# Kernel tuning notes

Measured on AMD Instinct MI355X. Metric: run time of the kernel, lower is better.

The kernel has to match this reference:

```python
import jax, jax.numpy as jnp
import numpy as np
from jax import lax

BN_EPS = 1e-5

def _conv(x, w, b, stride=2, pad=1):
    y = lax.conv_general_dilated(x, w, (stride, stride), [(pad, pad), (pad, pad)],
                                 dimension_numbers=('NCHW', 'OIHW', 'NCHW'))
    return y + b[None, :, None, None]

def _leaky(x):
    return jnp.where(x >= 0, x, 0.2 * x)

def setup_inputs() -> dict:
    key = jax.random.key(0)
    ks = jax.random.split(key, 10)
    B, C, S = 64, 3, 128
    flat = 128 * (S // 4) * (S // 4)  # 131072
    out_f, kdims = 100, 5
    def kaiming(k, shape, fan_in):
        bound = 1.0 / np.sqrt(fan_in)
        return jax.random.uniform(k, shape, jnp.float32, -bound, bound)
    x = jax.random.normal(ks[0], (B, C, S, S), jnp.float32)
    conv1_w = kaiming(ks[1], (64, C, 4, 4), C * 16)
    conv1_b = kaiming(ks[2], (64,), C * 16)
    conv2_w = kaiming(ks[3], (128, 64, 4, 4), 64 * 16)
    conv2_b = kaiming(ks[4], (128,), 64 * 16)
    bn_gamma = jnp.ones((128,), jnp.float32)
    bn_beta = jnp.zeros((128,), jnp.float32)
    T = jax.random.normal(ks[5], (flat, out_f, kdims), jnp.float32)  # N(0,1) init
    lin_w = kaiming(ks[6], (1, flat + out_f), flat + out_f)
    lin_b = kaiming(ks[7], (1,), flat + out_f)
    return {"x": x, "conv1_w": conv1_w, "conv1_b": conv1_b,
            "conv2_w": conv2_w, "conv2_b": conv2_b,
            "bn_gamma": bn_gamma, "bn_beta": bn_beta,
            "T": T, "lin_w": lin_w, "lin_b": lin_b}

def reference(x, conv1_w, conv1_b, conv2_w, conv2_b, bn_gamma, bn_beta, T, lin_w, lin_b):
    B = x.shape[0]
    h = _leaky(_conv(x, conv1_w, conv1_b))          # [B,64,S/2,S/2]
    h = _conv(h, conv2_w, conv2_b)                  # [B,128,S/4,S/4]
    mu = jnp.mean(h, axis=(0, 2, 3), keepdims=True)  # batchnorm (train mode, batch stats)
    var = jnp.mean((h - mu) ** 2, axis=(0, 2, 3), keepdims=True)
    h = (h - mu) * lax.rsqrt(var + BN_EPS)
    h = h * bn_gamma[None, :, None, None] + bn_beta[None, :, None, None]
    h = _leaky(h)
    feat = h.reshape(B, -1)                          # [B, flat]
    # minibatch discrimination
    M = (feat @ T.reshape(T.shape[0], -1)).reshape(B, T.shape[1], T.shape[2])  # [B,out,k]
    norm = jnp.abs(M[None, :, :, :] - M[:, None, :, :]).sum(3)  # [B,B,out] pairwise L1
    o_b = jnp.exp(-norm).sum(0)                      # [B,out]
    feat = jnp.concatenate([feat, o_b], axis=1)      # [B, flat+out]
    logits = feat @ lin_w.T + lin_b
    return jax.nn.sigmoid(logits)                    # [B,1]
```

## Files before the change

kernel.cpp:

```cpp
#include <hip/hip_runtime.h>
#include <hip/hip_bf16.h>
#include <math.h>

#define BB 64
#define SS 128
#define C1 64
#define H1D 64
#define C2 128
#define H2D 32
#define FLAT 131072
#define NCOL 500
#define KCH 256
#define KCSZ 512

typedef __attribute__((ext_vector_type(4))) float f32x4;
typedef __attribute__((ext_vector_type(8))) short bf16x8;

__device__ inline float bf2f(short s) {
    union { unsigned int u; float f; } z;
    z.u = ((unsigned int)(unsigned short)s) << 16;
    return z.f;
}

__global__ __launch_bounds__(256) void k_conv1p(const float* __restrict__ x,
    const float* __restrict__ w, const float* __restrict__ bias,
    const float* __restrict__ w2,
    __hip_bfloat16* __restrict__ h1, __hip_bfloat16* __restrict__ Bw)
{
    int bid = blockIdx.x;
    if (bid < 512) {
      int i = bid*256 + threadIdx.x;
      int jj = i & 7, oc = (i>>3)&127, kl8 = (i>>10)&31, stage = i>>15;
      int kl = kl8*8 + jj;
      int tap = kl >> 4, icl = kl & 15;
      int ic = stage*16 + icl;
      Bw[i] = __float2bfloat16(w2[(size_t)oc*1024 + ic*16 + tap]);
      return;
    }
    int tid = (bid - 512)*256 + threadIdx.x;
    int ow = tid & 63, oh = (tid>>6)&63, bi = tid>>12;
    int ih0 = oh*2-1, iw0 = ow*2-1;
    float in[48];
    #pragma unroll
    for (int ic=0; ic<3; ic++)
      #pragma unroll
      for (int kh=0; kh<4; kh++)
        #pragma unroll
        for (int kw=0; kw<4; kw++) {
          int ih = ih0+kh, iw = iw0+kw;
          float v = 0.f;
          if ((unsigned)ih < 128u && (unsigned)iw < 128u)
            v = x[((size_t)(bi*3+ic)*SS + ih)*SS + iw];
          in[ic*16+kh*4+kw] = v;
        }
    #pragma unroll
    for (int g=0; g<4; g++) {
      __hip_bfloat16 outv[16];
      #pragma unroll
      for (int ocl=0; ocl<16; ocl++) {
        int oc = g*16 + ocl;
        float a = bias[oc];
        const float* wp = w + oc*48;
        #pragma unroll
        for (int t=0; t<48; t++) a = fmaf(in[t], wp[t], a);
        a = a >= 0.f ? a : 0.2f*a;
        outv[ocl] = __float2bfloat16(a);
      }
      __hip_bfloat16* dst = h1 + (((size_t)g*BB + bi)*4096 + oh*64 + ow)*16;
      *(bf16x8*)(dst)     = *(bf16x8*)&outv[0];
      *(bf16x8*)(dst + 8) = *(bf16x8*)&outv[8];
    }
}

__global__ __launch_bounds__(256) void k_conv2(const __hip_bfloat16* __restrict__ h1,
    const __hip_bfloat16* __restrict__ Bw, const float* __restrict__ b2,
    __hip_bfloat16* __restrict__ h2b, double* __restrict__ bnp2)
{
    int bid = blockIdx.x;
    int nh = (bid >> 3) & 1;
    int pair = (bid >> 4)*8 + (bid & 7);
    int bi = pair >> 2, strip = pair & 3;
    int lane = threadIdx.x & 63, wv = threadIdx.x >> 6;
    int l15 = lane & 15, kg = lane >> 4;

    __shared__ __align__(16) short tile[36*33*24];
    __shared__ float2 bnl[4][16][16];

    f32x4 acc[4][4];
    #pragma unroll
    for (int m=0;m<4;m++)
      #pragma unroll
      for (int n=0;n<4;n++) acc[m][n] = (f32x4)(0.f);

    int ihb = strip*16 - 1;

    for (int stage=0; stage<4; ++stage) {
      const __hip_bfloat16* hsrc = h1 + ((size_t)stage*BB + bi)*4096*16;
      for (int idx = threadIdx.x; idx < 2376; idx += 256) {
        int half = idx & 1, p = idx >> 1;
        int ih_l = p / 66, iw_l = p - ih_l*66;
        int ih = ihb + ih_l, iw = iw_l - 1;
        int row48 = (ih_l*2 + (iw_l&1))*33 + (iw_l>>1);
        bf16x8 v = (bf16x8)(0);
        if ((unsigned)ih < 64u && (unsigned)iw < 64u)
          v = *(const bf16x8*)(hsrc + ((size_t)(ih*64+iw)*16 + half*8));
        *(bf16x8*)&tile[row48*24 + half*8] = v;
      }
      __syncthreads();
      const __hip_bfloat16* bwst = Bw + (size_t)stage*32*128*8;
      #pragma unroll
      for (int j=0; j<8; j++) {
        bf16x8 bf[4];
        #pragma unroll
        for (int nf=0; nf<4; nf++)
          bf[nf] = *(const bf16x8*)(bwst + ((size_t)((j*4+kg)*128) + nh*64 + nf*16 + l15)*8);
        int tap = 2*j + (kg>>1);
        int kh = tap>>2, kw = tap&3;
        int icl0 = (kg&1)*8;
        bf16x8 af[4];
        #pragma unroll
        for (int mf=0; mf<4; mf++) {
          int oh_l = 2*wv + (mf>>1);
          int ow   = (mf&1)*16 + l15;
          int ih_l = 2*oh_l + kh;
          int iw_l = 2*ow + kw;
          int row48 = (ih_l*2 + (iw_l&1))*33 + (iw_l>>1);
          af[mf] = *(const bf16x8*)&tile[row48*24 + icl0];
        }
        #pragma unroll
        for (int mf=0; mf<4; mf++)
          #pragma unroll
          for (int nf=0; nf<4; nf++)
            acc[mf][nf] = __builtin_amdgcn_mfma_f32_16x16x32_bf16(af[mf], bf[nf], acc[mf][nf], 0, 0, 0);
      }
      __syncthreads();
    }
    #pragma unroll
    for (int nf=0; nf<4; nf++) {
      int oc = nh*64 + nf*16 + l15;
      float bv = b2[oc];
      float s1 = 0.f, s2 = 0.f;
      #pragma unroll
      for (int mf=0; mf<4; mf++) {
        int p0 = wv*64 + mf*16 + kg*4;
        float v0 = acc[mf][nf][0] + bv;
        float v1 = acc[mf][nf][1] + bv;
        float v2 = acc[mf][nf][2] + bv;
        float v3 = acc[mf][nf][3] + bv;
        s1 += v0+v1+v2+v3;
        s2 = fmaf(v0,v0, fmaf(v1,v1, fmaf(v2,v2, fmaf(v3,v3, s2))));
        __hip_bfloat16 o4[4];
        o4[0] = __float2bfloat16(v0); o4[1] = __float2bfloat16(v1);
        o4[2] = __float2bfloat16(v2); o4[3] = __float2bfloat16(v3);
        *(double*)&h2b[((size_t)bi*C2 + oc)*1024 + strip*256 + p0] = *(double*)o4;
      }
      bnl[nf][wv*4+kg][l15] = make_float2(s1, s2);
    }
    __syncthreads();
    if (threadIdx.x < 64) {
      int nf = threadIdx.x >> 4, l = threadIdx.x & 15;
      double s1 = 0.0, s2 = 0.0;
      #pragma unroll
      for (int i=0;i<16;i++) {
        float2 v = bnl[nf][i][l];
        s1 += (double)v.x; s2 += (double)v.y;
      }
      int oc = nh*64 + nf*16 + l;
      bnp2[(size_t)oc*256 + pair]         = s1;
      bnp2[32768 + (size_t)oc*256 + pair] = s2;
    }
}

__global__ __launch_bounds__(256) void k_bnred(const double* __restrict__ bnp2,
    const float* __restrict__ gamma, const float* __restrict__ beta,
    float* __restrict__ stats)
{
    int c = blockIdx.x;
    int p = threadIdx.x;
    double s1 = bnp2[(size_t)c*256 + p];
    double s2 = bnp2[32768 + (size_t)c*256 + p];
    __shared__ double r1[256], r2[256];
    r1[p] = s1; r2[p] = s2;
    __syncthreads();
    for (int st = 128; st > 0; st >>= 1) {
      if (p < st) { r1[p] += r1[p+st]; r2[p] += r2[p+st]; }
      __syncthreads();
    }
    if (p == 0) {
      double mean = r1[0] * (1.0/65536.0);
      double var  = r2[0] * (1.0/65536.0) - mean*mean;
      double rstd = 1.0 / sqrt(var + 1e-5);
      double sc = rstd * (double)gamma[c];
      stats[c]       = (float)sc;
      stats[C2 + c]  = (float)((double)beta[c] - mean*sc);
    }
}

__global__ __launch_bounds__(256) void k_mgemm(const __hip_bfloat16* __restrict__ h2b,
    const float* __restrict__ stats, const float* __restrict__ T,
    __hip_bfloat16* __restrict__ Mpart)
{
    int t = threadIdx.x;
    int lane = t & 63, wv = t >> 6;
    int l15 = lane & 15, kg = lane >> 4;
    int bid = blockIdx.x;
    int xc = bid & 7, j = bid >> 3;
    int kc = xc*32 + (j >> 2);
    int ng = j & 3;
    int k0b = kc * KCSZ;

    int ch = kc >> 1;
    float sc = stats[ch], sh = stats[C2 + ch];

    __shared__ float Ts[2][32][134];

    int f4c = t & 31, rbase = t >> 5;
    int cols4 = ng*128 + f4c*4;
    bool cvalid = cols4 < 500;

    f32x4 acc[4][2];
    #pragma unroll
    for (int m=0;m<4;m++) { acc[m][0] = (f32x4)(0.f); acc[m][1] = (f32x4)(0.f); }

    float4 tv0, tv1, tv2, tv3;
    {
      int ks0 = k0b;
      tv0 = cvalid ? *(const float4*)&T[(size_t)(ks0+rbase   )*NCOL + cols4] : make_float4(0,0,0,0);
      tv1 = cvalid ? *(const float4*)&T[(size_t)(ks0+rbase+ 8)*NCOL + cols4] : make_float4(0,0,0,0);
      tv2 = cvalid ? *(const float4*)&T[(size_t)(ks0+rbase+16)*NCOL + cols4] : make_float4(0,0,0,0);
      tv3 = cvalid ? *(const float4*)&T[(size_t)(ks0+rbase+24)*NCOL + cols4] : make_float4(0,0,0,0);
      float* d0 = &Ts[0][rbase   ][f4c*4];
      float* d1 = &Ts[0][rbase+ 8][f4c*4];
      float* d2 = &Ts[0][rbase+16][f4c*4];
      float* d3 = &Ts[0][rbase+24][f4c*4];
      *(float2*)d0 = make_float2(tv0.x,tv0.y); *(float2*)(d0+2) = make_float2(tv0.z,tv0.w);
      *(float2*)d1 = make_float2(tv1.x,tv1.y); *(float2*)(d1+2) = make_float2(tv1.z,tv1.w);
      *(float2*)d2 = make_float2(tv2.x,tv2.y); *(float2*)(d2+2) = make_float2(tv2.z,tv2.w);
      *(float2*)d3 = make_float2(tv3.x,tv3.y); *(float2*)(d3+2) = make_float2(tv3.z,tv3.w);
    }
    __syncthreads();

    for (int s = 0; s < 16; s++) {
      int cur = s & 1;
      if (s < 15) {
        int ks0 = k0b + (s+1)*32;
        tv0 = cvalid ? *(const float4*)&T[(size_t)(ks0+rbase   )*NCOL + cols4] : make_float4(0,0,0,0);
        tv1 = cvalid ? *(const float4*)&T[(size_t)(ks0+rbase+ 8)*NCOL + cols4] : make_float4(0,0,0,0);
        tv2 = cvalid ? *(const float4*)&T[(size_t)(ks0+rbase+16)*NCOL + cols4] : make_float4(0,0,0,0);
        tv3 = cvalid ? *(const float4*)&T[(size_t)(ks0+rbase+24)*NCOL + cols4] : make_float4(0,0,0,0);
      }
      {
        int k0 = k0b + s*32;
        bf16x8 af[4];
        #pragma unroll
        for (int mf=0; mf<4; mf++) {
          bf16x8 raw = *(const bf16x8*)(h2b + (size_t)(mf*16 + l15)*FLAT + k0 + kg*8);
          __hip_bfloat16 ta[8];
          #pragma unroll
          for (int jj=0; jj<8; jj++) {
            float f = fmaf(bf2f(raw[jj]), sc, sh);
            f = f >= 0.f ? f : 0.2f*f;
            ta[jj] = __float2bfloat16(f);
          }
          af[mf] = *(bf16x8*)ta;
        }
        bf16x8 bfr[2];
        #pragma unroll
        for (int nf=0; nf<2; nf++) {
          int c = wv*32 + nf*16 + l15;
          __hip_bfloat16 tb[8];
          #pragma unroll
          for (int jj=0; jj<8; jj++)
            tb[jj] = __float2bfloat16(Ts[cur][kg*8+jj][c]);
          bfr[nf] = *(bf16x8*)tb;
        }
        #pragma unroll
        for (int mf=0;mf<4;mf++)
          #pragma unroll
          for (int nf=0;nf<2;nf++)
            acc[mf][nf] = __builtin_amdgcn_mfma_f32_16x16x32_bf16(af[mf], bfr[nf], acc[mf][nf], 0, 0, 0);
      }
      __syncthreads();
      if (s < 15) {
        int nb = cur ^ 1;
        float* d0 = &Ts[nb][rbase   ][f4c*4];
        float* d1 = &Ts[nb][rbase+ 8][f4c*4];
        float* d2 = &Ts[nb][rbase+16][f4c*4];
        float* d3 = &Ts[nb][rbase+24][f4c*4];
        *(float2*)d0 = make_float2(tv0.x,tv0.y); *(float2*)(d0+2) = make_float2(tv0.z,tv0.w);
        *(float2*)d1 = make_float2(tv1.x,tv1.y); *(float2*)(d1+2) = make_float2(tv1.z,tv1.w);
        *(float2*)d2 = make_float2(tv2.x,tv2.y); *(float2*)(d2+2) = make_float2(tv2.z,tv2.w);
        *(float2*)d3 = make_float2(tv3.x,tv3.y); *(float2*)(d3+2) = make_float2(tv3.z,tv3.w);
        __syncthreads();
      }
    }
    __hip_bfloat16* op = Mpart + (size_t)(kc*4 + ng)*8192;
    #pragma unroll
    for (int mf=0; mf<4; mf++) {
      __hip_bfloat16 buf[8];
      #pragma unroll
      for (int nf=0; nf<2; nf++)
        #pragma unroll
        for (int q=0; q<4; q++)
          buf[nf*4+q] = __float2bfloat16(acc[mf][nf][q]);
      *(bf16x8*)(op + ((size_t)mf*256 + t)*8) = *(bf16x8*)buf;
    }
}

__global__ __launch_bounds__(256) void k_mreduceA(const __hip_bfloat16* __restrict__ Mpart,
    float* __restrict__ Mpart2)
{
    int ng = blockIdx.x & 3, kg8 = blockIdx.x >> 2;
    int t = threadIdx.x;
    f32x4 a0[4], a1[4];
    #pragma unroll
    for (int mf=0; mf<4; mf++) { a0[mf] = (f32x4)(0.f); a1[mf] = (f32x4)(0.f); }
    #pragma unroll
    for (int kcl=0; kcl<8; kcl++) {
      int kc = kg8*8 + kcl;
      const __hip_bfloat16* ch = Mpart + (size_t)(kc*4 + ng)*8192;
      #pragma unroll
      for (int mf=0; mf<4; mf++) {
        bf16x8 v = *(const bf16x8*)(ch + ((size_t)mf*256 + t)*8);
        a0[mf][0] += bf2f(v[0]); a0[mf][1] += bf2f(v[1]);
        a0[mf][2] += bf2f(v[2]); a0[mf][3] += bf2f(v[3]);
        a1[mf][0] += bf2f(v[4]); a1[mf][1] += bf2f(v[5]);
        a1[mf][2] += bf2f(v[6]); a1[mf][3] += bf2f(v[7]);
      }
    }
    #pragma unroll
    for (int mf=0; mf<4; mf++) {
      float* dst = Mpart2 + ((size_t)(ng*32 + kg8)*4 + mf)*2048 + t*8;
      *(f32x4*)dst = a0[mf];
      *(f32x4*)(dst+4) = a1[mf];
    }
}

__global__ __launch_bounds__(256) void k_ob(const float* __restrict__ Mpart2,
    float* __restrict__ ob)
{
    int o = blockIdx.x;
    __shared__ float Ms[320];
    __shared__ float red[256];
    for (int idx = threadIdx.x; idx < 320; idx += 256) {
      int a = idx / 5, d = idx - a*5;
      int r = a, c = o*5 + d;
      int mf = r >> 4, kg = (r >> 2) & 3, q = r & 3;
      int ng = c >> 7, wv = (c >> 5) & 3, nf = (c >> 4) & 1, l15 = c & 15;
      int t = wv*64 + kg*16 + l15, j8 = nf*4 + q;
      const float* p = Mpart2 + ((size_t)(ng*32)*4 + mf)*2048 + t*8 + j8;
      float s = 0.f;
      #pragma unroll 8
      for (int kg8 = 0; kg8 < 32; kg8++) s += p[(size_t)kg8*8192];
      Ms[idx] = s;
    }
    __syncthreads();
    int b = threadIdx.x & 63, aq = threadIdx.x >> 6;
    float s = 0.f;
    for (int a = aq*16; a < aq*16+16; a++) {
      float n = 0.f;
      #pragma unroll
      for (int d=0; d<5; d++) n += fabsf(Ms[a*5+d] - Ms[b*5+d]);
      s += expf(-n);
    }
    red[threadIdx.x] = s;
    __syncthreads();
    if (threadIdx.x < 64)
      ob[(size_t)b*100 + o] = red[b] + red[64+b] + red[128+b] + red[192+b];
}

__global__ __launch_bounds__(256) void k_final1(const __hip_bfloat16* __restrict__ h2b,
    const float* __restrict__ stats, const float* __restrict__ lw,
    double* __restrict__ fpart)
{
    int bx = blockIdx.x;
    int b = bx >> 3, s = bx & 7;
    __shared__ float scs[16], shs[16];
    if (threadIdx.x < 16) {
      scs[threadIdx.x] = stats[s*16 + threadIdx.x];
      shs[threadIdx.x] = stats[C2 + s*16 + threadIdx.x];
    }
    __syncthreads();
    const __hip_bfloat16* hp = h2b + (size_t)b*FLAT;
    double acc = 0.0;
    for (int g = s*2048 + threadIdx.x; g < (s+1)*2048; g += 256) {
      int k = g*8;
      int cl = (k >> 10) & 15;
      float sc = scs[cl], sh = shs[cl];
      bf16x8 v = *(const bf16x8*)&hp[k];
      float4 w0 = *(const float4*)&lw[k];
      float4 w1 = *(const float4*)&lw[k+4];
      float f0 = fmaf(bf2f(v[0]), sc, sh); f0 = f0>=0.f?f0:0.2f*f0;
      float f1 = fmaf(bf2f(v[1]), sc, sh); f1 = f1>=0.f?f1:0.2f*f1;
      float f2 = fmaf(bf2f(v[2]), sc, sh); f2 = f2>=0.f?f2:0.2f*f2;
      float f3 = fmaf(bf2f(v[3]), sc, sh); f3 = f3>=0.f?f3:0.2f*f3;
      float f4 = fmaf(bf2f(v[4]), sc, sh); f4 = f4>=0.f?f4:0.2f*f4;
      float f5 = fmaf(bf2f(v[5]), sc, sh); f5 = f5>=0.f?f5:0.2f*f5;
      float f6 = fmaf(bf2f(v[6]), sc, sh); f6 = f6>=0.f?f6:0.2f*f6;
      float f7 = fmaf(bf2f(v[7]), sc, sh); f7 = f7>=0.f?f7:0.2f*f7;
      acc = fma((double)f0, (double)w0.x, acc);
      acc = fma((double)f1, (double)w0.y, acc);
      acc = fma((double)f2, (double)w0.z, acc);
      acc = fma((double)f3, (double)w0.w, acc);
      acc = fma((double)f4, (double)w1.x, acc);
      acc = fma((double)f5, (double)w1.y, acc);
      acc = fma((double)f6, (double)w1.z, acc);
      acc = fma((double)f7, (double)w1.w, acc);
    }
    __shared__ double red[256];
    red[threadIdx.x] = acc;
    __syncthreads();
    for (int st = 128; st > 0; st >>= 1) {
      if (threadIdx.x < st) red[threadIdx.x] += red[threadIdx.x + st];
      __syncthreads();
    }
    if (threadIdx.x == 0) fpart[bx] = red[0];
}

__global__ void k_final2(const double* __restrict__ fpart,
    const float* __restrict__ ob, const float* __restrict__ lw,
    const float* __restrict__ lb, float* __restrict__ out)
{
    int b = threadIdx.x;
    double s = 0.0;
    #pragma unroll
    for (int i = 0; i < 8; i++) s += fpart[b*8 + i];
    for (int o = 0; o < 100; o++)
      s = fma((double)ob[(size_t)b*100 + o], (double)lw[FLAT + o], s);
    s += (double)lb[0];
    out[b] = (float)(1.0 / (1.0 + exp(-s)));
}

extern "C" void kernel_launch(void* const* d_in, const int* in_sizes, int n_in,
                              void* d_out, int out_size, void* d_ws, size_t ws_size,
                              hipStream_t stream)
{
    const float* x   = (const float*)d_in[0];
    const float* w1  = (const float*)d_in[1];
    const float* b1  = (const float*)d_in[2];
    const float* w2  = (const float*)d_in[3];
    const float* b2  = (const float*)d_in[4];
    const float* gam = (const float*)d_in[5];
    const float* bet = (const float*)d_in[6];
    const float* T   = (const float*)d_in[7];
    const float* lw  = (const float*)d_in[8];
    const float* lb  = (const float*)d_in[9];
    float* out = (float*)d_out;

    float* ws = (float*)d_ws;
    __hip_bfloat16* h1 = (__hip_bfloat16*)ws;
    __hip_bfloat16* Mpart = (__hip_bfloat16*)ws;
    __hip_bfloat16* h2b = (__hip_bfloat16*)(ws + 8388608);
    __hip_bfloat16* Bw  = (__hip_bfloat16*)(ws + 12582912);
    float* stats = ws + 12648448;
    float* ob    = ws + 12648704;
    float* Mpart2 = ws + 12655104;
    double* bnp2  = (double*)(ws + 13703680);
    double* fpart = (double*)(ws + 13834752);

    k_conv1p<<<1536, 256, 0, stream>>>(x, w1, b1, w2, h1, Bw);
    k_conv2<<<512, 256, 0, stream>>>(h1, Bw, b2, h2b, bnp2);
    k_bnred<<<128, 256, 0, stream>>>(bnp2, gam, bet, stats);
    k_mgemm<<<1024, 256, 0, stream>>>(h2b, stats, T, Mpart);
    k_mreduceA<<<128, 256, 0, stream>>>(Mpart, Mpart2);
    k_ob<<<100, 256, 0, stream>>>(Mpart2, ob);
    k_final1<<<512, 256, 0, stream>>>(h2b, stats, lw, fpart);
    k_final2<<<1, 64, 0, stream>>>(fpart, ob, lw, lb, out);
}
```

Measured before the change: 167.8 us.

## Fuse BN stats reduction, M-GEMM and linear partials into one launch

Drops the separate BN-reduction and final-linear kernels. Each M-GEMM block now recomputes its channel's batch statistics from the partial sums, and 512 extra blocks in the same grid compute the linear-layer partial dot products, each with its own BN stats. This removes two launches and the serial dependency between them, and lets the linear partials run alongside the GEMM. In exchange, the BN reduction is done redundantly in every block, and the fused kernel uses more shared memory.

After: 168.4 us, median of 2. Within noise of the previous version (+0.3%).

```diff
diff --git a/kernel.cpp b/kernel.cpp
--- a/kernel.cpp
+++ b/kernel.cpp
@@ -171,219 +171,179 @@
     }
 }
 
-__global__ __launch_bounds__(256) void k_bnred(const double* __restrict__ bnp2,
-    const float* __restrict__ gamma, const float* __restrict__ beta,
-    float* __restrict__ stats)
-{
-    int c = blockIdx.x;
-    int p = threadIdx.x;
-    double s1 = bnp2[(size_t)c*256 + p];
-    double s2 = bnp2[32768 + (size_t)c*256 + p];
-    __shared__ double r1[256], r2[256];
-    r1[p] = s1; r2[p] = s2;
-    __syncthreads();
-    for (int st = 128; st > 0; st >>= 1) {
-      if (p < st) { r1[p] += r1[p+st]; r2[p] += r2[p+st]; }
-      __syncthreads();
-    }
-    if (p == 0) {
-      double mean = r1[0] * (1.0/65536.0);
-      double var  = r2[0] * (1.0/65536.0) - mean*mean;
-      double rstd = 1.0 / sqrt(var + 1e-5);
-      double sc = rstd * (double)gamma[c];
-      stats[c]       = (float)sc;
-      stats[C2 + c]  = (float)((double)beta[c] - mean*sc);
-    }
-}
-
-__global__ __launch_bounds__(256) void k_mgemm(const __hip_bfloat16* __restrict__ h2b,
-    const float* __restrict__ stats, const float* __restrict__ T,
-    __hip_bfloat16* __restrict__ Mpart)
-{
+__global__ __launch_bounds__(256) void k_mgf(const __hip_bfloat16* __restrict__ h2b,
+    const double* __restrict__ bnp2, const float* __restrict__ gamma,
+    const float* __restrict__ beta, const float* __restrict__ T,
+    const float* __restrict__ lw,
+    __hip_bfloat16* __restrict__ Mpart, double* __restrict__ fpart)
+{
+    __shared__ __align__(16) char smem[38432];
     int t = threadIdx.x;
-    int lane = t & 63, wv = t >> 6;
-    int l15 = lane & 15, kg = lane >> 4;
     int bid = blockIdx.x;
-    int xc = bid & 7, j = bid >> 3;
-    int kc = xc*32 + (j >> 2);
-    int ng = j & 3;
-    int k0b = kc * KCSZ;
-
-    int ch = kc >> 1;
-    float sc = stats[ch], sh = stats[C2 + ch];
-
-    __shared__ float Ts[2][32][134];
-
-    int f4c = t & 31, rbase = t >> 5;
-    int cols4 = ng*128 + f4c*4;
-    bool cvalid = cols4 < 500;
-
-    f32x4 acc[4][2];
-    #pragma unroll
-    for (int m=0;m<4;m++) { acc[m][0] = (f32x4)(0.f); acc[m][1] = (f32x4)(0.f); }
-
-    float4 tv0, tv1, tv2, tv3;
-    {
-      int ks0 = k0b;
-      tv0 = cvalid ? *(const float4*)&T[(size_t)(ks0+rbase   )*NCOL + cols4] : make_float4(0,0,0,0);
-      tv1 = cvalid ? *(const float4*)&T[(size_t)(ks0+rbase+ 8)*NCOL + cols4] : make_float4(0,0,0,0);
-      tv2 = cvalid ? *(const float4*)&T[(size_t)(ks0+rbase+16)*NCOL + cols4] : make_float4(0,0,0,0);
-      tv3 = cvalid ? *(const float4*)&T[(size_t)(ks0+rbase+24)*NCOL + cols4] : make_float4(0,0,0,0);
-      float* d0 = &Ts[0][rbase   ][f4c*4];
-      float* d1 = &Ts[0][rbase+ 8][f4c*4];
-      float* d2 = &Ts[0][rbase+16][f4c*4];
-      float* d3 = &Ts[0][rbase+24][f4c*4];
-      *(float2*)d0 = make_float2(tv0.x,tv0.y); *(float2*)(d0+2) = make_float2(tv0.z,tv0.w);
-      *(float2*)d1 = make_float2(tv1.x,tv1.y); *(float2*)(d1+2) = make_float2(tv1.z,tv1.w);
-      *(float2*)d2 = make_float2(tv2.x,tv2.y); *(float2*)(d2+2) = make_float2(tv2.z,tv2.w);
-      *(float2*)d3 = make_float2(tv3.x,tv3.y); *(float2*)(d3+2) = make_float2(tv3.z,tv3.w);
-    }
-    __syncthreads();
-
-    for (int s = 0; s < 16; s++) {
-      int cur = s & 1;
-      if (s < 15) {
-        int ks0 = k0b + (s+1)*32;
+
+    if (bid < 1024) {
+      int lane = t & 63, wv = t >> 6;
+      int l15 = lane & 15, kg = lane >> 4;
+      int xc = bid & 7, j = bid >> 3;
+      int kc = xc*32 + (j >> 2);
+      int ng = j & 3;
+      int k0b = kc * KCSZ;
+      int ch = kc >> 1;
+
+      double* r1 = (double*)(smem + 34304);
+      double* r2 = (double*)(smem + 34304 + 2048);
+      float*  stf = (float*)(smem + 34304 + 4096);
+      r1[t] = bnp2[(size_t)ch*256 + t];
+      r2[t] = bnp2[32768 + (size_t)ch*256 + t];
+      __syncthreads();
+      for (int st = 128; st > 0; st >>= 1) {
+        if (t < st) { r1[t] += r1[t+st]; r2[t] += r2[t+st]; }
+        __syncthreads();
+      }
+      if (t == 0) {
+        double mean = r1[0] * (1.0/65536.0);
+        double var  = r2[0] * (1.0/65536.0) - mean*mean;
+        double rstd = 1.0 / sqrt(var + 1e-5);
+        double scd  = rstd * (double)gamma[ch];
+        stf[0] = (float)scd;
+        stf[1] = (float)((double)beta[ch] - mean*scd);
+      }
+      __syncthreads();
+      float sc = stf[0], sh = stf[1];
+
+      typedef float TsRow[134];
+      TsRow* Ts0 = (TsRow*)smem;
+      TsRow* Ts1 = (TsRow*)(smem + 32*134*4);
+
+      int f4c = t & 31, rbase = t >> 5;
+      int cols4 = ng*128 + f4c*4;
+      bool cvalid = cols4 < 500;
+
+      f32x4 acc[4][2];
+      #pragma unroll
+      for (int m=0;m<4;m++) { acc[m][0] = (f32x4)(0.f); acc[m][1] = (f32x4)(0.f); }
+
+      float4 tv0, tv1, tv2, tv3;
+      {
+        int ks0 = k0b;
         tv0 = cvalid ? *(const float4*)&T[(size_t)(ks0+rbase   )*NCOL + cols4] : make_float4(0,0,0,0);
         tv1 = cvalid ? *(const float4*)&T[(size_t)(ks0+rbase+ 8)*NCOL + cols4] : make_float4(0,0,0,0);
         tv2 = cvalid ? *(const float4*)&T[(size_t)(ks0+rbase+16)*NCOL + cols4] : make_float4(0,0,0,0);
         tv3 = cvalid ? *(const float4*)&T[(size_t)(ks0+rbase+24)*NCOL + cols4] : make_float4(0,0,0,0);
-      }
-      {
-        int k0 = k0b + s*32;
-        bf16x8 af[4];
-        #pragma unroll
-        for (int mf=0; mf<4; mf++) {
-          bf16x8 raw = *(const bf16x8*)(h2b + (size_t)(mf*16 + l15)*FLAT + k0 + kg*8);
-          __hip_bfloat16 ta[8];
-          #pragma unroll
-          for (int jj=0; jj<8; jj++) {
-            float f = fmaf(bf2f(raw[jj]), sc, sh);
-            f = f >= 0.f ? f : 0.2f*f;
-            ta[jj] = __float2bfloat16(f);
-          }
-          af[mf] = *(bf16x8*)ta;
-        }
-        bf16x8 bfr[2];
-        #pragma unroll
-        for (int nf=0; nf<2; nf++) {
-          int c = wv*32 + nf*16 + l15;
-          __hip_bfloat16 tb[8];
-          #pragma unroll
-          for (int jj=0; jj<8; jj++)
-            tb[jj] = __float2bfloat16(Ts[cur][kg*8+jj][c]);
-          bfr[nf] = *(bf16x8*)tb;
-        }
-        #pragma unroll
-        for (int mf=0;mf<4;mf++)
-          #pragma unroll
-          for (int nf=0;nf<2;nf++)
-            acc[mf][nf] = __builtin_amdgcn_mfma_f32_16x16x32_bf16(af[mf], bfr[nf], acc[mf][nf], 0, 0, 0);
-      }
-      __syncthreads();
-      if (s < 15) {
-        int nb = cur ^ 1;
-        float* d0 = &Ts[nb][rbase   ][f4c*4];
-        float* d1 = &Ts[nb][rbase+ 8][f4c*4];
-        float* d2 = &Ts[nb][rbase+16][f4c*4];
-        float* d3 = &Ts[nb][rbase+24][f4c*4];
+        float* d0 = &Ts0[rbase   ][f4c*4];
+        float* d1 = &Ts0[rbase+ 8][f4c*4];
+        float* d2 = &Ts0[rbase+16][f4c*4];
+        float* d3 = &Ts0[rbase+24][f4c*4];
         *(float2*)d0 = make_float2(tv0.x,tv0.y); *(float2*)(d0+2) = make_float2(tv0.z,tv0.w);
         *(float2*)d1 = make_float2(tv1.x,tv1.y); *(float2*)(d1+2) = make_float2(tv1.z,tv1.w);
         *(float2*)d2 = make_float2(tv2.x,tv2.y); *(float2*)(d2+2) = make_float2(tv2.z,tv2.w);
         *(float2*)d3 = make_float2(tv3.x,tv3.y); *(float2*)(d3+2) = make_float2(tv3.z,tv3.w);
+      }
+      __syncthreads();
+
+      for (int s = 0; s < 16; s++) {
+        TsRow* Tc = (s & 1) ? Ts1 : Ts0;
+        TsRow* Tn = (s & 1) ? Ts0 : Ts1;
+        if (s < 15) {
+          int ks0 = k0b + (s+1)*32;
+          tv0 = cvalid ? *(const float4*)&T[(size_t)(ks0+rbase   )*NCOL + cols4] : make_float4(0,0,0,0);
+          tv1 = cvalid ? *(const float4*)&T[(size_t)(ks0+rbase+ 8)*NCOL + cols4] : make_float4(0,0,0,0);
+          tv2 = cvalid ? *(const float4*)&T[(size_t)(ks0+rbase+16)*NCOL + cols4] : make_float4(0,0,0,0);
+          tv3 = cvalid ? *(const float4*)&T[(size_t)(ks0+rbase+24)*NCOL + cols4] : make_float4(0,0,0,0);
+        }
+        {
+          int k0 = k0b + s*32;
+          bf16x8 af[4];
+          #pragma unroll
+          for (int mf=0; mf<4; mf++) {
+            bf16x8 raw = *(const bf16x8*)(h2b + (size_t)(mf*16 + l15)*FLAT + k0 + kg*8);
+            __hip_bfloat16 ta[8];
+            #pragma unroll
+            for (int jj=0; jj<8; jj++) {
+              float f = fmaf(bf2f(raw[jj]), sc, sh);
+              f = f >= 0.f ? f : 0.2f*f;
+              ta[jj] = __float2bfloat16(f);
+            }
+            af[mf] = *(bf16x8*)ta;
+          }
+          bf16x8 bfr[2];
+          #pragma unroll
+          for (int nf=0; nf<2; nf++) {
+            int c = wv*32 + nf*16 + l15;
+            __hip_bfloat16 tb[8];
+            #pragma unroll
+            for (int jj=0; jj<8; jj++)
+              tb[jj] = __float2bfloat16(Tc[kg*8+jj][c]);
+            bfr[nf] = *(bf16x8*)tb;
+          }
+          #pragma unroll
+          for (int mf=0;mf<4;mf++)
+            #pragma unroll
+            for (int nf=0;nf<2;nf++)
+              acc[mf][nf] = __builtin_amdgcn_mfma_f32_16x16x32_bf16(af[mf], bfr[nf], acc[mf][nf], 0, 0, 0);
+        }
         __syncthreads();
-      }
-    }
-    __hip_bfloat16* op = Mpart + (size_t)(kc*4 + ng)*8192;
-    #pragma unroll
-    for (int mf=0; mf<4; mf++) {
-      __hip_bfloat16 buf[8];
-      #pragma unroll
-      for (int nf=0; nf<2; nf++)
-        #pragma unroll
-        for (int q=0; q<4; q++)
-          buf[nf*4+q] = __float2bfloat16(acc[mf][nf][q]);
-      *(bf16x8*)(op + ((size_t)mf*256 + t)*8) = *(bf16x8*)buf;
-    }
-}
-
-__global__ __launch_bounds__(256) void k_mreduceA(const __hip_bfloat16* __restrict__ Mpart,
-    float* __restrict__ Mpart2)
-{
-    int ng = blockIdx.x & 3, kg8 = blockIdx.x >> 2;
-    int t = threadIdx.x;
-    f32x4 a0[4], a1[4];
-    #pragma unroll
-    for (int mf=0; mf<4; mf++) { a0[mf] = (f32x4)(0.f); a1[mf] = (f32x4)(0.f); }
-    #pragma unroll
-    for (int kcl=0; kcl<8; kcl++) {
-      int kc = kg8*8 + kcl;
-      const __hip_bfloat16* ch = Mpart + (size_t)(kc*4 + ng)*8192;
+        if (s < 15) {
+          float* d0 = &Tn[rbase   ][f4c*4];
+          float* d1 = &Tn[rbase+ 8][f4c*4];
+          float* d2 = &Tn[rbase+16][f4c*4];
+          float* d3 = &Tn[rbase+24][f4c*4];
+          *(float2*)d0 = make_float2(tv0.x,tv0.y); *(float2*)(d0+2) = make_float2(tv0.z,tv0.w);
+          *(float2*)d1 = make_float2(tv1.x,tv1.y); *(float2*)(d1+2) = make_float2(tv1.z,tv1.w);
+          *(float2*)d2 = make_float2(tv2.x,tv2.y); *(float2*)(d2+2) = make_float2(tv2.z,tv2.w);
+          *(float2*)d3 = make_float2(tv3.x,tv3.y); *(float2*)(d3+2) = make_float2(tv3.z,tv3.w);
+          __syncthreads();
+        }
+      }
+      __hip_bfloat16* op = Mpart + (size_t)(kc*4 + ng)*8192;
       #pragma unroll
       for (int mf=0; mf<4; mf++) {
-        bf16x8 v = *(const bf16x8*)(ch + ((size_t)mf*256 + t)*8);
-        a0[mf][0] += bf2f(v[0]); a0[mf][1] += bf2f(v[1]);
-        a0[mf][2] += bf2f(v[2]); a0[mf][3] += bf2f(v[3]);
-        a1[mf][0] += bf2f(v[4]); a1[mf][1] += bf2f(v[5]);
-        a1[mf][2] += bf2f(v[6]); a1[mf][3] += bf2f(v[7]);
-      }
-    }
-    #pragma unroll
-    for (int mf=0; mf<4; mf++) {
-      float* dst = Mpart2 + ((size_t)(ng*32 + kg8)*4 + mf)*2048 + t*8;
-      *(f32x4*)dst = a0[mf];
-      *(f32x4*)(dst+4) = a1[mf];
-    }
-}
-
-__global__ __launch_bounds__(256) void k_ob(const float* __restrict__ Mpart2,
-    float* __restrict__ ob)
-{
-    int o = blockIdx.x;
-    __shared__ float Ms[320];
-    __shared__ float red[256];
-    for (int idx = threadIdx.x; idx < 320; idx += 256) {
-      int a = idx / 5, d = idx - a*5;
-      int r = a, c = o*5 + d;
-      int mf = r >> 4, kg = (r >> 2) & 3, q = r & 3;
-      int ng = c >> 7, wv = (c >> 5) & 3, nf = (c >> 4) & 1, l15 = c & 15;
-      int t = wv*64 + kg*16 + l15, j8 = nf*4 + q;
-      const float* p = Mpart2 + ((size_t)(ng*32)*4 + mf)*2048 + t*8 + j8;
-      float s = 0.f;
-      #pragma unroll 8
-      for (int kg8 = 0; kg8 < 32; kg8++) s += p[(size_t)kg8*8192];
-      Ms[idx] = s;
-    }
-    __syncthreads();
-    int b = threadIdx.x & 63, aq = threadIdx.x >> 6;
-    float s = 0.f;
-    for (int a = aq*16; a < aq*16+16; a++) {
-      float n = 0.f;
-      #pragma unroll
-      for (int d=0; d<5; d++) n += fabsf(Ms[a*5+d] - Ms[b*5+d]);
-      s += expf(-n);
-    }
-    red[threadIdx.x] = s;
-    __syncthreads();
-    if (threadIdx.x < 64)
-      ob[(size_t)b*100 + o] = red[b] + red[64+b] + red[128+b] + red[192+b];
-}
-
-__global__ __launch_bounds__(256) void k_final1(const __hip_bfloat16* __restrict__ h2b,
-    const float* __restrict__ stats, const float* __restrict__ lw,
-    double* __restrict__ fpart)
-{
-    int bx = blockIdx.x;
+        __hip_bfloat16 buf[8];
+        #pragma unroll
+        for (int nf=0; nf<2; nf++)
+          #pragma unroll
+          for (int q=0; q<4; q++)
+            buf[nf*4+q] = __float2bfloat16(acc[mf][nf][q]);
+        *(bf16x8*)(op + ((size_t)mf*256 + t)*8) = *(bf16x8*)buf;
+      }
+      return;
+    }
+
+    int bx = bid - 1024;
     int b = bx >> 3, s = bx & 7;
-    __shared__ float scs[16], shs[16];
-    if (threadIdx.x < 16) {
-      scs[threadIdx.x] = stats[s*16 + threadIdx.x];
-      shs[threadIdx.x] = stats[C2 + s*16 + threadIdx.x];
-    }
-    __syncthreads();
+    double* rA = (double*)smem;
+    double* rB = (double*)(smem + 2048);
+    float*  scs = (float*)(smem + 4096);
+    float*  shs = (float*)(smem + 4096 + 64);
+    double* red = (double*)(smem + 8192);
+    {
+      int cl = t >> 4, i = t & 15;
+      int c = s*16 + cl;
+      double a1 = 0.0, a2 = 0.0;
+      #pragma unroll
+      for (int q=0;q<16;q++) {
+        a1 += bnp2[(size_t)c*256 + i*16 + q];
+        a2 += bnp2[32768 + (size_t)c*256 + i*16 + q];
+      }
+      rA[cl*16+i] = a1; rB[cl*16+i] = a2;
+      __syncthreads();
+      for (int st = 8; st > 0; st >>= 1) {
+        if (i < st) { rA[cl*16+i] += rA[cl*16+i+st]; rB[cl*16+i] += rB[cl*16+i+st]; }
+        __syncthreads();
+      }
+      if (i == 0) {
+        double mean = rA[cl*16] * (1.0/65536.0);
+        double var  = rB[cl*16] * (1.0/65536.0) - mean*mean;
+        double rstd = 1.0 / sqrt(var + 1e-5);
+        double scd  = rstd * (double)gamma[c];
+        scs[cl] = (float)scd;
+        shs[cl] = (float)((double)beta[c] - mean*scd);
+      }
+      __syncthreads();
+    }
     const __hip_bfloat16* hp = h2b + (size_t)b*FLAT;
     double acc = 0.0;
-    for (int g = s*2048 + threadIdx.x; g < (s+1)*2048; g += 256) {
+    for (int g = s*2048 + t; g < (s+1)*2048; g += 256) {
       int k = g*8;
       int cl = (k >> 10) & 15;
       float sc = scs[cl], sh = shs[cl];
@@ -407,14 +367,75 @@
       acc = fma((double)f6, (double)w1.z, acc);
       acc = fma((double)f7, (double)w1.w, acc);
     }
-    __shared__ double red[256];
-    red[threadIdx.x] = acc;
+    red[t] = acc;
     __syncthreads();
     for (int st = 128; st > 0; st >>= 1) {
-      if (threadIdx.x < st) red[threadIdx.x] += red[threadIdx.x + st];
-      __syncthreads();
-    }
-    if (threadIdx.x == 0) fpart[bx] = red[0];
+      if (t < st) red[t] += red[t + st];
+      __syncthreads();
+    }
+    if (t == 0) fpart[bx] = red[0];
+}
+
+__global__ __launch_bounds__(256) void k_mreduceA(const __hip_bfloat16* __restrict__ Mpart,
+    float* __restrict__ Mpart2)
+{
+    int ng = blockIdx.x & 3, kg8 = blockIdx.x >> 2;
+    int t = threadIdx.x;
+    f32x4 a0[4], a1[4];
+    #pragma unroll
+    for (int mf=0; mf<4; mf++) { a0[mf] = (f32x4)(0.f); a1[mf] = (f32x4)(0.f); }
+    #pragma unroll
+    for (int kcl=0; kcl<8; kcl++) {
+      int kc = kg8*8 + kcl;
+      const __hip_bfloat16* ch = Mpart + (size_t)(kc*4 + ng)*8192;
+      #pragma unroll
+      for (int mf=0; mf<4; mf++) {
+        bf16x8 v = *(const bf16x8*)(ch + ((size_t)mf*256 + t)*8);
+        a0[mf][0] += bf2f(v[0]); a0[mf][1] += bf2f(v[1]);
+        a0[mf][2] += bf2f(v[2]); a0[mf][3] += bf2f(v[3]);
+        a1[mf][0] += bf2f(v[4]); a1[mf][1] += bf2f(v[5]);
+        a1[mf][2] += bf2f(v[6]); a1[mf][3] += bf2f(v[7]);
+      }
+    }
+    #pragma unroll
+    for (int mf=0; mf<4; mf++) {
+      float* dst = Mpart2 + ((size_t)(ng*32 + kg8)*4 + mf)*2048 + t*8;
+      *(f32x4*)dst = a0[mf];
+      *(f32x4*)(dst+4) = a1[mf];
+    }
+}
+
+__global__ __launch_bounds__(256) void k_ob(const float* __restrict__ Mpart2,
+    float* __restrict__ ob)
+{
+    int o = blockIdx.x;
+    __shared__ float Ms[320];
+    __shared__ float red[256];
+    for (int idx = threadIdx.x; idx < 320; idx += 256) {
+      int a = idx / 5, d = idx - a*5;
+      int r = a, c = o*5 + d;
+      int mf = r >> 4, kg = (r >> 2) & 3, q = r & 3;
+      int ng = c >> 7, wv = (c >> 5) & 3, nf = (c >> 4) & 1, l15 = c & 15;
+      int t = wv*64 + kg*16 + l15, j8 = nf*4 + q;
+      const float* p = Mpart2 + ((size_t)(ng*32)*4 + mf)*2048 + t*8 + j8;
+      float s = 0.f;
+      #pragma unroll 8
+      for (int kg8 = 0; kg8 < 32; kg8++) s += p[(size_t)kg8*8192];
+      Ms[idx] = s;
+    }
+    __syncthreads();
+    int b = threadIdx.x & 63, aq = threadIdx.x >> 6;
+    float s = 0.f;
+    for (int a = aq*16; a < aq*16+16; a++) {
+      float n = 0.f;
+      #pragma unroll
+      for (int d=0; d<5; d++) n += fabsf(Ms[a*5+d] - Ms[b*5+d]);
+      s += expf(-n);
+    }
+    red[threadIdx.x] = s;
+    __syncthreads();
+    if (threadIdx.x < 64)
+      ob[(size_t)b*100 + o] = red[b] + red[64+b] + red[128+b] + red[192+b];
 }
 
 __global__ void k_final2(const double* __restrict__ fpart,
@@ -452,7 +473,6 @@
     __hip_bfloat16* Mpart = (__hip_bfloat16*)ws;
     __hip_bfloat16* h2b = (__hip_bfloat16*)(ws + 8388608);
     __hip_bfloat16* Bw  = (__hip_bfloat16*)(ws + 12582912);
-    float* stats = ws + 12648448;
     float* ob    = ws + 12648704;
     float* Mpart2 = ws + 12655104;
     double* bnp2  = (double*)(ws + 13703680);
@@ -460,10 +480,8 @@
 
     k_conv1p<<<1536, 256, 0, stream>>>(x, w1, b1, w2, h1, Bw);
     k_conv2<<<512, 256, 0, stream>>>(h1, Bw, b2, h2b, bnp2);
-    k_bnred<<<128, 256, 0, stream>>>(bnp2, gam, bet, stats);
-    k_mgemm<<<1024, 256, 0, stream>>>(h2b, stats, T, Mpart);
+    k_mgf<<<1536, 256, 0, stream>>>(h2b, bnp2, gam, bet, T, lw, Mpart, fpart);
     k_mreduceA<<<128, 256, 0, stream>>>(Mpart, Mpart2);
     k_ob<<<100, 256, 0, stream>>>(Mpart2, ob);
-    k_final1<<<512, 256, 0, stream>>>(h2b, stats, lw, fpart);
     k_final2<<<1, 64, 0, stream>>>(fpart, ob, lw, lb, out);
 }
```
